# Performance work log

Hardware: AMD Instinct MI355X
Metric: run time of the kernel (lower is better)

Reference implementation:

```python
import jax, jax.numpy as jnp
import numpy as np

WS = 7          # window size
NH = 12         # num heads
DIM = 384       # embed dim
HD = DIM // NH  # head dim
BW = 2048       # B_ = batch * num_windows
N = WS * WS     # tokens per window


def _relative_position_index(ws):
    coords = np.stack(np.meshgrid(np.arange(ws), np.arange(ws), indexing='ij'))  # [2,ws,ws]
    cf = coords.reshape(2, -1)                      # [2, ws*ws]
    rel = cf[:, :, None] - cf[:, None, :]           # [2, N, N]
    rel = rel.transpose(1, 2, 0).copy()             # [N, N, 2]
    rel[:, :, 0] += ws - 1
    rel[:, :, 1] += ws - 1
    rel[:, :, 0] *= 2 * ws - 1
    return jnp.asarray(rel.sum(-1))                 # [N, N] int


REL_IDX = _relative_position_index(WS)


def setup_inputs() -> dict:
    key = jax.random.key(0)
    ks = jax.random.split(key, 6)
    return {
        'x': jax.random.normal(ks[0], (BW, N, DIM), dtype=jnp.float32),
        'qkv_w': jax.random.normal(ks[1], (3 * DIM, DIM), dtype=jnp.float32) * 0.02,
        'qkv_b': jax.random.normal(ks[2], (3 * DIM,), dtype=jnp.float32) * 0.02,
        'proj_w': jax.random.normal(ks[3], (DIM, DIM), dtype=jnp.float32) * 0.02,
        'proj_b': jax.random.normal(ks[4], (DIM,), dtype=jnp.float32) * 0.02,
        'rel_bias_table': jax.random.normal(ks[5], ((2 * WS - 1) ** 2, NH), dtype=jnp.float32) * 0.02,
    }


def reference(x, qkv_w, qkv_b, proj_w, proj_b, rel_bias_table):
    B_, n, c = x.shape
    scale = HD ** -0.5
    qkv = x @ qkv_w.T + qkv_b                                   # [B_, N, 3*DIM]
    qkv = qkv.reshape(B_, n, 3, NH, HD).transpose(2, 0, 3, 1, 4)  # [3, B_, H, N, HD]
    q, k, v = qkv[0], qkv[1], qkv[2]
    attn = jnp.einsum('bhnd,bhmd->bhnm', q * scale, k)           # [B_, H, N, N]
    bias = rel_bias_table[REL_IDX.reshape(-1)].reshape(n, n, NH)  # gather -> [N, N, H]
    attn = attn + bias.transpose(2, 0, 1)[None]                   # add [1, H, N, N]
    attn = jax.nn.softmax(attn, axis=-1)
    out = jnp.einsum('bhnm,bhmd->bhnd', attn, v)                 # [B_, H, N, HD]
    out = out.transpose(0, 2, 1, 3).reshape(B_, n, c)            # [B_, N, C]
    return out @ proj_w.T + proj_b
```

## Files before the change

### kernel.cpp

```cpp
#include <hip/hip_runtime.h>
#include <hip/hip_bf16.h>

#define NH 12
constexpr float SCALE = 0.17677669529663687f;
constexpr int TOKENS = 100352;

using f32x4  = __attribute__((ext_vector_type(4))) float;
using bf16x8 = __attribute__((ext_vector_type(8))) __bf16;

__device__ inline void gload_lds16(const void* g, void* l) {
  __builtin_amdgcn_global_load_lds(
      (const __attribute__((address_space(1))) void*)g,
      (__attribute__((address_space(3))) void*)l, 16, 0, 0);
}

__device__ inline bf16x8 cvt8(float4 a, float4 b) {
  bf16x8 o;
  o[0] = (__bf16)a.x; o[1] = (__bf16)a.y; o[2] = (__bf16)a.z; o[3] = (__bf16)a.w;
  o[4] = (__bf16)b.x; o[5] = (__bf16)b.y; o[6] = (__bf16)b.z; o[7] = (__bf16)b.w;
  return o;
}

#define MFMA(a, b, c) __builtin_amdgcn_mfma_f32_16x16x32_bf16(a, b, c, 0, 0, 0)

__global__ __launch_bounds__(256) void wa_prep(
    const float* __restrict__ qkv_w, const float* __restrict__ proj_w,
    const float* __restrict__ tbl,
    __bf16* __restrict__ qkv_w_bf, __bf16* __restrict__ proj_w_bf,
    float* __restrict__ biasTt) {
  int p = blockIdx.x * 256 + threadIdx.x;
  if (p < 442368) { qkv_w_bf[p] = (__bf16)qkv_w[p]; return; }
  p -= 442368;
  if (p < 147456) { proj_w_bf[p] = (__bf16)proj_w[p]; return; }
  p -= 147456;
  if (p >= 49152) return;
  int h = p >> 12, rem = p & 4095, j = rem >> 6, i = rem & 63;
  float v;
  if (j >= 49) v = -1e30f;
  else if (i >= 49) v = 0.0f;
  else {
    int py = i / 7, px = i % 7, qy = j / 7, qx = j % 7;
    v = tbl[((py - qy + 6) * 13 + (px - qx + 6)) * NH + h];
  }
  biasTt[p] = v;
}

__global__ __launch_bounds__(256, 4) void wa_qkv(
    const float* __restrict__ x, const __bf16* __restrict__ wq,
    const float* __restrict__ qkv_b, __bf16* __restrict__ qkv) {
  __shared__ alignas(16) __bf16 smem[12288];
  __bf16* As = smem;
  __bf16* Bs = smem + 4096;
  __bf16* Cs = smem + 4096;
  const int t = threadIdx.x, lane = t & 63, wv = t >> 6;
  const int lr = lane & 15, ls = lane >> 4;
  const int bid = blockIdx.x;
  const int q = bid / 72, rem = bid - q * 72;
  const int nb = rem >> 3, mb = q * 8 + (rem & 7);
  const int wr = wv >> 1, wc = wv & 1;
  f32x4 acc[2][4] = {};
  for (int kk = 0; kk < 6; ++kk) {
    if (kk) __syncthreads();
    float4 a0[2], a1[2];
    int rowA[2], cA[2];
    #pragma unroll
    for (int j = 0; j < 2; ++j) {
      int p = j * 256 + t;
      rowA[j] = p >> 3; cA[j] = p & 7;
      const float* src = x + (size_t)(mb * 64 + rowA[j]) * 384 + kk * 64 + cA[j] * 8;
      a0[j] = *(const float4*)src;
      a1[j] = *(const float4*)(src + 4);
    }
    #pragma unroll
    for (int j = 0; j < 4; ++j) {
      int p = j * 256 + t;
      int c = p >> 3, sl = p & 7;
      gload_lds16(wq + (size_t)(nb * 128 + c) * 384 + kk * 64 + (sl ^ (c & 7)) * 8,
                  Bs + p * 8);
    }
    #pragma unroll
    for (int j = 0; j < 2; ++j) {
      int cw = cA[j] ^ (rowA[j] & 7);
      *(bf16x8*)(As + rowA[j] * 64 + cw * 8) = cvt8(a0[j], a1[j]);
    }
    __syncthreads();
    #pragma unroll
    for (int ks = 0; ks < 2; ++ks) {
      bf16x8 af[2], bfr[4];
      #pragma unroll
      for (int rt = 0; rt < 2; ++rt) {
        int row = wr * 32 + rt * 16 + lr;
        af[rt] = *(const bf16x8*)(As + row * 64 + (((ks * 4 + ls) ^ (row & 7)) * 8));
      }
      #pragma unroll
      for (int ct = 0; ct < 4; ++ct) {
        int c = wc * 64 + ct * 16 + lr;
        bfr[ct] = *(const bf16x8*)(Bs + c * 64 + (((ks * 4 + ls) ^ (c & 7)) * 8));
      }
      #pragma unroll
      for (int rt = 0; rt < 2; ++rt)
        #pragma unroll
        for (int ct = 0; ct < 4; ++ct)
          acc[rt][ct] = MFMA(af[rt], bfr[ct], acc[rt][ct]);
    }
  }
  __syncthreads();
  #pragma unroll
  for (int ct = 0; ct < 4; ++ct) {
    float b = qkv_b[nb * 128 + wc * 64 + ct * 16 + lr];
    #pragma unroll
    for (int rt = 0; rt < 2; ++rt)
      #pragma unroll
      for (int r = 0; r < 4; ++r) {
        int row = wr * 32 + rt * 16 + ls * 4 + r;
        Cs[row * 128 + wc * 64 + ct * 16 + lr] = (__bf16)(acc[rt][ct][r] + b);
      }
  }
  __syncthreads();
  #pragma unroll
  for (int j = 0; j < 4; ++j) {
    int p = j * 256 + t;
    int row = p >> 4, sub = p & 15;
    *(bf16x8*)(qkv + (size_t)(mb * 64 + row) * 1152 + nb * 128 + sub * 8) =
        *(const bf16x8*)(Cs + p * 8);
  }
}

__global__ __launch_bounds__(256, 3) void wa_attn(
    const float* __restrict__ biasTt, __bf16* __restrict__ qkv) {
  __shared__ __bf16 Pbuf[4][4096];
  __shared__ __bf16 Vbuf[4][2048];
  const int t = threadIdx.x, lane = t & 63, wv = t >> 6;
  const int lr = lane & 15, ls = lane >> 4;
  const int pair = blockIdx.x * 4 + wv;
  const int w = pair / NH, h = pair - w * NH;
  const int w49 = w * 49;
  __bf16* Pw = Pbuf[wv];
  __bf16* Vw = Vbuf[wv];
  f32x4 zero = {0.f, 0.f, 0.f, 0.f};
  bf16x8 ones;
  #pragma unroll
  for (int e = 0; e < 8; ++e) ones[e] = (__bf16)1.0f;

  {
    int row = lane;
    int tok = w49 + (row < 49 ? row : 48);
    const bf16x8* vsrc = (const bf16x8*)(qkv + (size_t)tok * 1152 + 768 + h * 32);
    int f = (row & 3) ^ ((row >> 3) & 3);
    #pragma unroll
    for (int c = 0; c < 4; ++c)
      *(bf16x8*)(Vw + row * 32 + ((c ^ f) * 8)) = vsrc[c];
  }
  bf16x8 qa[4], kb[4];
  #pragma unroll
  for (int rt = 0; rt < 4; ++rt) {
    int tok = min(w49 + rt * 16 + lr, TOKENS - 1);
    qa[rt] = *(const bf16x8*)(qkv + (size_t)tok * 1152 + h * 32 + ls * 8);
  }
  #pragma unroll
  for (int ct = 0; ct < 4; ++ct) {
    int tok = min(w49 + ct * 16 + lr, TOKENS - 1);
    kb[ct] = *(const bf16x8*)(qkv + (size_t)tok * 1152 + 384 + h * 32 + ls * 8);
  }
  f32x4 sacc[4][4];
  #pragma unroll
  for (int rt = 0; rt < 4; ++rt)
    #pragma unroll
    for (int ct = 0; ct < 4; ++ct)
      sacc[rt][ct] = MFMA(qa[rt], kb[ct], zero);
  #pragma unroll
  for (int rt = 0; rt < 4; ++rt) {
    int row0 = rt * 16 + ls * 4;
    #pragma unroll
    for (int ct = 0; ct < 4; ++ct) {
      int col = ct * 16 + lr;
      float4 bias = *(const float4*)(biasTt + (size_t)(h * 64 + col) * 64 + row0);
      #pragma unroll
      for (int r = 0; r < 4; ++r) {
        int row = row0 + r;
        float pr = __expf(fmaf(sacc[rt][ct][r], SCALE, ((const float*)&bias)[r]));
        Pw[row * 64 + (((col >> 3) ^ (row & 7)) * 8) + (col & 7)] = (__bf16)pr;
      }
    }
  }
  f32x4 oacc[4][2] = {};
  f32x4 osum[4] = {zero, zero, zero, zero};
  #pragma unroll
  for (int ks = 0; ks < 2; ++ks) {
    bf16x8 vb0, vb1;
    #pragma unroll
    for (int e = 0; e < 8; ++e) {
      int j = ks * 32 + ls * 8 + e;
      int a = j * 32 + (((lr >> 3) ^ (e & 3) ^ ls) * 8) + (lr & 7);
      vb0[e] = Vw[a];
      vb1[e] = Vw[a ^ 16];
    }
    #pragma unroll
    for (int rt = 0; rt < 4; ++rt) {
      int row = rt * 16 + lr;
      bf16x8 pa = *(const bf16x8*)(Pw + row * 64 + (((ks * 4 + ls) ^ (row & 7)) * 8));
      oacc[rt][0] = MFMA(pa, vb0, oacc[rt][0]);
      oacc[rt][1] = MFMA(pa, vb1, oacc[rt][1]);
      osum[rt]    = MFMA(pa, ones, osum[rt]);
    }
  }
  #pragma unroll
  for (int rt = 0; rt < 4; ++rt)
    #pragma unroll
    for (int r = 0; r < 4; ++r) {
      int row = rt * 16 + ls * 4 + r;
      if (row < 49) {
        float inv = 1.0f / osum[rt][r];
        __bf16* o = qkv + (size_t)(w49 + row) * 1152 + h * 32;
        o[lr]      = (__bf16)(oacc[rt][0][r] * inv);
        o[16 + lr] = (__bf16)(oacc[rt][1][r] * inv);
      }
    }
}

__global__ __launch_bounds__(256, 4) void wa_proj(
    const __bf16* __restrict__ qkv, const __bf16* __restrict__ pw,
    const float* __restrict__ proj_b, float* __restrict__ out) {
  __shared__ alignas(16) __bf16 As[64 * 64];
  __shared__ alignas(16) __bf16 Bs[128 * 64];
  const int t = threadIdx.x, lane = t & 63, wv = t >> 6;
  const int lr = lane & 15, ls = lane >> 4;
  const int bid = blockIdx.x;
  const int q = bid / 24, rem = bid - q * 24;
  const int nb = rem >> 3, mb = q * 8 + (rem & 7);
  const int wr = wv >> 1, wc = wv & 1;
  f32x4 acc[2][4] = {};
  for (int kk = 0; kk < 6; ++kk) {
    if (kk) __syncthreads();
    #pragma unroll
    for (int j = 0; j < 2; ++j) {
      int p = j * 256 + t;
      int row = p >> 3, sl = p & 7;
      gload_lds16(qkv + (size_t)(mb * 64 + row) * 1152 + kk * 64 + (sl ^ (row & 7)) * 8,
                  As + p * 8);
    }
    #pragma unroll
    for (int j = 0; j < 4; ++j) {
      int p = j * 256 + t;
      int c = p >> 3, sl = p & 7;
      gload_lds16(pw + (size_t)(nb * 128 + c) * 384 + kk * 64 + (sl ^ (c & 7)) * 8,
                  Bs + p * 8);
    }
    __syncthreads();
    #pragma unroll
    for (int ks = 0; ks < 2; ++ks) {
      bf16x8 af[2], bfr[4];
      #pragma unroll
      for (int rt = 0; rt < 2; ++rt) {
        int row = wr * 32 + rt * 16 + lr;
        af[rt] = *(const bf16x8*)(As + row * 64 + (((ks * 4 + ls) ^ (row & 7)) * 8));
      }
      #pragma unroll
      for (int ct = 0; ct < 4; ++ct) {
        int c = wc * 64 + ct * 16 + lr;
        bfr[ct] = *(const bf16x8*)(Bs + c * 64 + (((ks * 4 + ls) ^ (c & 7)) * 8));
      }
      #pragma unroll
      for (int rt = 0; rt < 2; ++rt)
        #pragma unroll
        for (int ct = 0; ct < 4; ++ct)
          acc[rt][ct] = MFMA(af[rt], bfr[ct], acc[rt][ct]);
    }
  }
  #pragma unroll
  for (int ct = 0; ct < 4; ++ct) {
    int col = nb * 128 + wc * 64 + ct * 16 + lr;
    float b = proj_b[col];
    #pragma unroll
    for (int rt = 0; rt < 2; ++rt)
      #pragma unroll
      for (int r = 0; r < 4; ++r) {
        int row = wr * 32 + rt * 16 + ls * 4 + r;
        out[(size_t)(mb * 64 + row) * 384 + col] = acc[rt][ct][r] + b;
      }
  }
}

extern "C" void kernel_launch(void* const* d_in, const int* in_sizes, int n_in,
                              void* d_out, int out_size, void* d_ws, size_t ws_size,
                              hipStream_t stream) {
  const float* x      = (const float*)d_in[0];
  const float* qkv_w  = (const float*)d_in[1];
  const float* qkv_b  = (const float*)d_in[2];
  const float* proj_w = (const float*)d_in[3];
  const float* proj_b = (const float*)d_in[4];
  const float* tbl    = (const float*)d_in[5];
  float* out = (float*)d_out;

  char* ws = (char*)d_ws;
  __bf16* qkv_w_bf  = (__bf16*)ws;
  __bf16* proj_w_bf = (__bf16*)(ws + 884736);
  float*  biasTt    = (float*)(ws + 1179648);
  __bf16* qkv_buf   = (__bf16*)(ws + 1376256);

  wa_prep<<<2496, 256, 0, stream>>>(qkv_w, proj_w, tbl, qkv_w_bf, proj_w_bf, biasTt);
  wa_qkv<<<14112, 256, 0, stream>>>(x, qkv_w_bf, qkv_b, qkv_buf);
  wa_attn<<<6144, 256, 0, stream>>>(biasTt, qkv_buf);
  wa_proj<<<4704, 256, 0, stream>>>(qkv_buf, proj_w_bf, proj_b, out);
}
```

Baseline: 327.3 us.

## Double-buffer LDS tiles in QKV and projection GEMMs to overlap loads with MFMA

Both GEMM kernels now use ping-pong LDS buffers (48 KB). The loads for the next K-slice are issued before the current slice's MFMAs run, so global-memory latency can overlap with compute and there is one barrier per iteration instead of two. In exchange, shared memory per block doubles and launch bounds drop from 4 to 3 blocks per CU, which lowers occupancy. The QKV kernel keeps the x tile in registers across the compute phase, which raises register pressure.

```diff
diff --git a/kernel.cpp b/kernel.cpp
--- a/kernel.cpp
+++ b/kernel.cpp
@@ -45,45 +45,63 @@
   biasTt[p] = v;
 }
 
-__global__ __launch_bounds__(256, 4) void wa_qkv(
+__global__ __launch_bounds__(256, 3) void wa_qkv(
     const float* __restrict__ x, const __bf16* __restrict__ wq,
     const float* __restrict__ qkv_b, __bf16* __restrict__ qkv) {
-  __shared__ alignas(16) __bf16 smem[12288];
-  __bf16* As = smem;
-  __bf16* Bs = smem + 4096;
-  __bf16* Cs = smem + 4096;
+  __shared__ alignas(16) __bf16 smem[24576];
   const int t = threadIdx.x, lane = t & 63, wv = t >> 6;
   const int lr = lane & 15, ls = lane >> 4;
   const int bid = blockIdx.x;
   const int q = bid / 72, rem = bid - q * 72;
   const int nb = rem >> 3, mb = q * 8 + (rem & 7);
   const int wr = wv >> 1, wc = wv & 1;
-  f32x4 acc[2][4] = {};
-  for (int kk = 0; kk < 6; ++kk) {
-    if (kk) __syncthreads();
-    float4 a0[2], a1[2];
-    int rowA[2], cA[2];
+
+  int rowA[2], cA[2];
+  #pragma unroll
+  for (int j = 0; j < 2; ++j) {
+    int p = j * 256 + t;
+    rowA[j] = p >> 3; cA[j] = p & 7;
+  }
+  float4 a0[2], a1[2];
+  auto issueA = [&](int kk) {
     #pragma unroll
     for (int j = 0; j < 2; ++j) {
-      int p = j * 256 + t;
-      rowA[j] = p >> 3; cA[j] = p & 7;
       const float* src = x + (size_t)(mb * 64 + rowA[j]) * 384 + kk * 64 + cA[j] * 8;
       a0[j] = *(const float4*)src;
       a1[j] = *(const float4*)(src + 4);
     }
+  };
+  auto writeA = [&](__bf16* Asp) {
+    #pragma unroll
+    for (int j = 0; j < 2; ++j) {
+      int cw = cA[j] ^ (rowA[j] & 7);
+      *(bf16x8*)(Asp + rowA[j] * 64 + cw * 8) = cvt8(a0[j], a1[j]);
+    }
+  };
+  auto issueB = [&](int kk, __bf16* Bsp) {
     #pragma unroll
     for (int j = 0; j < 4; ++j) {
       int p = j * 256 + t;
       int c = p >> 3, sl = p & 7;
       gload_lds16(wq + (size_t)(nb * 128 + c) * 384 + kk * 64 + (sl ^ (c & 7)) * 8,
-                  Bs + p * 8);
-    }
-    #pragma unroll
-    for (int j = 0; j < 2; ++j) {
-      int cw = cA[j] ^ (rowA[j] & 7);
-      *(bf16x8*)(As + rowA[j] * 64 + cw * 8) = cvt8(a0[j], a1[j]);
-    }
-    __syncthreads();
+                  Bsp + p * 8);
+    }
+  };
+
+  f32x4 acc[2][4] = {};
+  issueA(0);
+  issueB(0, smem + 8192);
+  writeA(smem);
+  __syncthreads();
+
+  for (int kk = 0; kk < 6; ++kk) {
+    const int p = kk & 1;
+    __bf16* As = smem + p * 4096;
+    __bf16* Bs = smem + 8192 + p * 8192;
+    if (kk < 5) {
+      issueA(kk + 1);
+      issueB(kk + 1, smem + 8192 + (p ^ 1) * 8192);
+    }
     #pragma unroll
     for (int ks = 0; ks < 2; ++ks) {
       bf16x8 af[2], bfr[4];
@@ -103,8 +121,10 @@
         for (int ct = 0; ct < 4; ++ct)
           acc[rt][ct] = MFMA(af[rt], bfr[ct], acc[rt][ct]);
     }
-  }
-  __syncthreads();
+    if (kk < 5) writeA(smem + (p ^ 1) * 4096);
+    __syncthreads();
+  }
+  __bf16* Cs = smem + 8192;
   #pragma unroll
   for (int ct = 0; ct < 4; ++ct) {
     float b = qkv_b[nb * 128 + wc * 64 + ct * 16 + lr];
@@ -218,35 +238,49 @@
     }
 }
 
-__global__ __launch_bounds__(256, 4) void wa_proj(
+__global__ __launch_bounds__(256, 3) void wa_proj(
     const __bf16* __restrict__ qkv, const __bf16* __restrict__ pw,
     const float* __restrict__ proj_b, float* __restrict__ out) {
-  __shared__ alignas(16) __bf16 As[64 * 64];
-  __shared__ alignas(16) __bf16 Bs[128 * 64];
+  __shared__ alignas(16) __bf16 smem[24576];
   const int t = threadIdx.x, lane = t & 63, wv = t >> 6;
   const int lr = lane & 15, ls = lane >> 4;
   const int bid = blockIdx.x;
   const int q = bid / 24, rem = bid - q * 24;
   const int nb = rem >> 3, mb = q * 8 + (rem & 7);
   const int wr = wv >> 1, wc = wv & 1;
-  f32x4 acc[2][4] = {};
-  for (int kk = 0; kk < 6; ++kk) {
-    if (kk) __syncthreads();
+
+  auto issueA = [&](int kk, __bf16* Asp) {
     #pragma unroll
     for (int j = 0; j < 2; ++j) {
       int p = j * 256 + t;
       int row = p >> 3, sl = p & 7;
       gload_lds16(qkv + (size_t)(mb * 64 + row) * 1152 + kk * 64 + (sl ^ (row & 7)) * 8,
-                  As + p * 8);
-    }
+                  Asp + p * 8);
+    }
+  };
+  auto issueB = [&](int kk, __bf16* Bsp) {
     #pragma unroll
     for (int j = 0; j < 4; ++j) {
       int p = j * 256 + t;
       int c = p >> 3, sl = p & 7;
       gload_lds16(pw + (size_t)(nb * 128 + c) * 384 + kk * 64 + (sl ^ (c & 7)) * 8,
-                  Bs + p * 8);
-    }
-    __syncthreads();
+                  Bsp + p * 8);
+    }
+  };
+
+  f32x4 acc[2][4] = {};
+  issueA(0, smem);
+  issueB(0, smem + 8192);
+  __syncthreads();
+
+  for (int kk = 0; kk < 6; ++kk) {
+    const int p = kk & 1;
+    __bf16* As = smem + p * 4096;
+    __bf16* Bs = smem + 8192 + p * 8192;
+    if (kk < 5) {
+      issueA(kk + 1, smem + (p ^ 1) * 4096);
+      issueB(kk + 1, smem + 8192 + (p ^ 1) * 8192);
+    }
     #pragma unroll
     for (int ks = 0; ks < 2; ++ks) {
       bf16x8 af[2], bfr[4];
@@ -266,6 +300,7 @@
         for (int ct = 0; ct < 4; ++ct)
           acc[rt][ct] = MFMA(af[rt], bfr[ct], acc[rt][ct]);
     }
+    __syncthreads();
   }
   #pragma unroll
   for (int ct = 0; ct < 4; ++ct) {
```

Result: slower. 375.0 us (+14.6%).

## Enlarge QKV GEMM tile to 128x128 and use 32x32x16 MFMA

Applied to the files above, without the earlier changes.

The QKV projection kernel now computes a 128-row by 128-column output tile per block instead of 64x128, halving the grid, and switches from 16x16x32 to 32x32x16 bf16 MFMA with 2x2 accumulator tiles per wave. Each weight tile loaded into LDS is reused across twice as many rows, and the larger MFMA shape needs fewer fragment loads per FLOP. In exchange, LDS per block grows to 32 KB and accumulator register use rises, which may lower occupancy under the 4-block launch bound.

```diff
diff --git a/kernel.cpp b/kernel.cpp
--- a/kernel.cpp
+++ b/kernel.cpp
@@ -6,6 +6,7 @@
 constexpr int TOKENS = 100352;
 
 using f32x4  = __attribute__((ext_vector_type(4))) float;
+using f32x16 = __attribute__((ext_vector_type(16))) float;
 using bf16x8 = __attribute__((ext_vector_type(8))) __bf16;
 
 __device__ inline void gload_lds16(const void* g, void* l) {
@@ -21,7 +22,8 @@
   return o;
 }
 
-#define MFMA(a, b, c) __builtin_amdgcn_mfma_f32_16x16x32_bf16(a, b, c, 0, 0, 0)
+#define MFMA(a, b, c)   __builtin_amdgcn_mfma_f32_16x16x32_bf16(a, b, c, 0, 0, 0)
+#define MFMA32(a, b, c) __builtin_amdgcn_mfma_f32_32x32x16_bf16(a, b, c, 0, 0, 0)
 
 __global__ __launch_bounds__(256) void wa_prep(
     const float* __restrict__ qkv_w, const float* __restrict__ proj_w,
@@ -48,80 +50,81 @@
 __global__ __launch_bounds__(256, 4) void wa_qkv(
     const float* __restrict__ x, const __bf16* __restrict__ wq,
     const float* __restrict__ qkv_b, __bf16* __restrict__ qkv) {
-  __shared__ alignas(16) __bf16 smem[12288];
+  __shared__ alignas(16) __bf16 smem[16384];
   __bf16* As = smem;
-  __bf16* Bs = smem + 4096;
-  __bf16* Cs = smem + 4096;
+  __bf16* Bs = smem + 8192;
+  __bf16* Cs = smem;
   const int t = threadIdx.x, lane = t & 63, wv = t >> 6;
-  const int lr = lane & 15, ls = lane >> 4;
+  const int l31 = lane & 31, hi = lane >> 5;
   const int bid = blockIdx.x;
   const int q = bid / 72, rem = bid - q * 72;
   const int nb = rem >> 3, mb = q * 8 + (rem & 7);
   const int wr = wv >> 1, wc = wv & 1;
-  f32x4 acc[2][4] = {};
+
+  f32x16 acc[2][2] = {};
   for (int kk = 0; kk < 6; ++kk) {
     if (kk) __syncthreads();
-    float4 a0[2], a1[2];
-    int rowA[2], cA[2];
-    #pragma unroll
-    for (int j = 0; j < 2; ++j) {
+    float4 a0[4], a1[4];
+    int rowA[4], cA[4];
+    #pragma unroll
+    for (int j = 0; j < 4; ++j) {
       int p = j * 256 + t;
       rowA[j] = p >> 3; cA[j] = p & 7;
-      const float* src = x + (size_t)(mb * 64 + rowA[j]) * 384 + kk * 64 + cA[j] * 8;
+      const float* src = x + (size_t)(mb * 128 + rowA[j]) * 384 + kk * 64 + cA[j] * 8;
       a0[j] = *(const float4*)src;
       a1[j] = *(const float4*)(src + 4);
     }
     #pragma unroll
     for (int j = 0; j < 4; ++j) {
       int p = j * 256 + t;
-      int c = p >> 3, sl = p & 7;
-      gload_lds16(wq + (size_t)(nb * 128 + c) * 384 + kk * 64 + (sl ^ (c & 7)) * 8,
+      int row = p >> 3, c = p & 7;
+      gload_lds16(wq + (size_t)(nb * 128 + row) * 384 + kk * 64 + (c ^ (row & 7)) * 8,
                   Bs + p * 8);
     }
     #pragma unroll
-    for (int j = 0; j < 2; ++j) {
-      int cw = cA[j] ^ (rowA[j] & 7);
-      *(bf16x8*)(As + rowA[j] * 64 + cw * 8) = cvt8(a0[j], a1[j]);
-    }
+    for (int j = 0; j < 4; ++j)
+      *(bf16x8*)(As + rowA[j] * 64 + ((cA[j] ^ (rowA[j] & 7)) * 8)) = cvt8(a0[j], a1[j]);
     __syncthreads();
     #pragma unroll
-    for (int ks = 0; ks < 2; ++ks) {
-      bf16x8 af[2], bfr[4];
+    for (int ksn = 0; ksn < 4; ++ksn) {
+      int ch = ksn * 2 + hi;
+      bf16x8 af[2], bfr[2];
       #pragma unroll
       for (int rt = 0; rt < 2; ++rt) {
-        int row = wr * 32 + rt * 16 + lr;
-        af[rt] = *(const bf16x8*)(As + row * 64 + (((ks * 4 + ls) ^ (row & 7)) * 8));
-      }
-      #pragma unroll
-      for (int ct = 0; ct < 4; ++ct) {
-        int c = wc * 64 + ct * 16 + lr;
-        bfr[ct] = *(const bf16x8*)(Bs + c * 64 + (((ks * 4 + ls) ^ (c & 7)) * 8));
+        int row = wr * 64 + rt * 32 + l31;
+        af[rt] = *(const bf16x8*)(As + row * 64 + ((ch ^ (row & 7)) * 8));
+      }
+      #pragma unroll
+      for (int ct = 0; ct < 2; ++ct) {
+        int col = wc * 64 + ct * 32 + l31;
+        bfr[ct] = *(const bf16x8*)(Bs + col * 64 + ((ch ^ (col & 7)) * 8));
       }
       #pragma unroll
       for (int rt = 0; rt < 2; ++rt)
         #pragma unroll
-        for (int ct = 0; ct < 4; ++ct)
-          acc[rt][ct] = MFMA(af[rt], bfr[ct], acc[rt][ct]);
+        for (int ct = 0; ct < 2; ++ct)
+          acc[rt][ct] = MFMA32(af[rt], bfr[ct], acc[rt][ct]);
     }
   }
   __syncthreads();
-  #pragma unroll
-  for (int ct = 0; ct < 4; ++ct) {
-    float b = qkv_b[nb * 128 + wc * 64 + ct * 16 + lr];
-    #pragma unroll
-    for (int rt = 0; rt < 2; ++rt)
-      #pragma unroll
-      for (int r = 0; r < 4; ++r) {
-        int row = wr * 32 + rt * 16 + ls * 4 + r;
-        Cs[row * 128 + wc * 64 + ct * 16 + lr] = (__bf16)(acc[rt][ct][r] + b);
-      }
-  }
+  float bias[2];
+  #pragma unroll
+  for (int ct = 0; ct < 2; ++ct) bias[ct] = qkv_b[nb * 128 + wc * 64 + ct * 32 + l31];
+  #pragma unroll
+  for (int rt = 0; rt < 2; ++rt)
+    #pragma unroll
+    for (int ct = 0; ct < 2; ++ct)
+      #pragma unroll
+      for (int reg = 0; reg < 16; ++reg) {
+        int row = wr * 64 + rt * 32 + (reg & 3) + 4 * hi + 8 * (reg >> 2);
+        Cs[row * 128 + wc * 64 + ct * 32 + l31] = (__bf16)(acc[rt][ct][reg] + bias[ct]);
+      }
   __syncthreads();
   #pragma unroll
-  for (int j = 0; j < 4; ++j) {
+  for (int j = 0; j < 8; ++j) {
     int p = j * 256 + t;
     int row = p >> 4, sub = p & 15;
-    *(bf16x8*)(qkv + (size_t)(mb * 64 + row) * 1152 + nb * 128 + sub * 8) =
+    *(bf16x8*)(qkv + (size_t)(mb * 128 + row) * 1152 + nb * 128 + sub * 8) =
         *(const bf16x8*)(Cs + p * 8);
   }
 }
@@ -299,7 +302,7 @@
   __bf16* qkv_buf   = (__bf16*)(ws + 1376256);
 
   wa_prep<<<2496, 256, 0, stream>>>(qkv_w, proj_w, tbl, qkv_w_bf, proj_w_bf, biasTt);
-  wa_qkv<<<14112, 256, 0, stream>>>(x, qkv_w_bf, qkv_b, qkv_buf);
+  wa_qkv<<<7056, 256, 0, stream>>>(x, qkv_w_bf, qkv_b, qkv_buf);
   wa_attn<<<6144, 256, 0, stream>>>(biasTt, qkv_buf);
   wa_proj<<<4704, 256, 0, stream>>>(qkv_buf, proj_w_bf, proj_b, out);
 }
```

New measurement: 352.9 us. 1.08x slower.
